# Kernel tuning notes

Hardware: AMD Instinct MI355X
Metric: run time of the kernel (lower is better)

The kernel has to match this reference:

```python
import jax, jax.numpy as jnp
import numpy as np

DIM_MODEL = 2048
DQK = 64
DV = 64
NUM_HEADS = 32
NUM_GROUPS = 8
H_PER_G = NUM_HEADS // NUM_GROUPS
ROPE_THETA = 10000.0
RMS_EPS = 1e-6


def _rope(x):
    # x: [b, g, h, s, d]; rotate-half RoPE over last dim, positions along s.
    d = x.shape[-1]
    s = x.shape[-2]
    inv_freq = 1.0 / (ROPE_THETA ** (jnp.arange(0, d, 2, dtype=jnp.float32) / d))  # [d/2]
    ang = jnp.arange(s, dtype=jnp.float32)[:, None] * inv_freq[None, :]  # [s, d/2]
    cos, sin = jnp.cos(ang), jnp.sin(ang)
    x1, x2 = x[..., : d // 2], x[..., d // 2 :]
    return jnp.concatenate([x1 * cos - x2 * sin, x2 * cos + x1 * sin], axis=-1)


def setup_inputs() -> dict:
    key = jax.random.key(0)
    k1, k2, k3 = jax.random.split(key, 3)
    b, s = 2, 2048
    concat = NUM_HEADS * DQK + NUM_GROUPS * (DQK + DV)  # 3072
    x = jax.random.normal(k1, (b, s, DIM_MODEL), dtype=jnp.float32)
    w_in = jax.random.normal(k2, (concat, DIM_MODEL), dtype=jnp.float32) * (DIM_MODEL ** -0.5)
    w_out = jax.random.normal(k3, (DIM_MODEL, NUM_HEADS * DV), dtype=jnp.float32) * ((NUM_HEADS * DV) ** -0.5)
    rms_w = jnp.ones((DIM_MODEL,), dtype=jnp.float32)
    return {"x": x, "w_in": w_in, "w_out": w_out, "rms_w": rms_w}


def reference(x, w_in, w_out, rms_w):
    b, s, _ = x.shape
    # RMSNorm
    y = x * jax.lax.rsqrt(jnp.mean(x * x, axis=-1, keepdims=True) + RMS_EPS) * rms_w
    # In-projection (Linear, no bias): y @ w_in.T
    y = jnp.einsum('bsm,cm->bsc', y, w_in)
    cq = NUM_HEADS * DQK
    ck = NUM_GROUPS * DQK
    q, k, v = y[..., :cq], y[..., cq:cq + ck], y[..., cq + ck:]
    # q: b s (g h d) -> b g h s d ; k,v: b s (g d) -> b g 1 s d
    q = q.reshape(b, s, NUM_GROUPS, H_PER_G, DQK).transpose(0, 2, 3, 1, 4)
    k = k.reshape(b, s, NUM_GROUPS, DQK).transpose(0, 2, 1, 3)[:, :, None]
    v = v.reshape(b, s, NUM_GROUPS, DV).transpose(0, 2, 1, 3)[:, :, None]
    q = _rope(q)
    k = _rope(k)
    # scores with GQA broadcast over h
    qk = jnp.einsum('bghsd,bgxpd->bghsp', q, k) * (DQK ** -0.5)
    causal = jnp.tril(jnp.ones((s, s), dtype=bool))
    qk = jnp.where(causal, qk, -jnp.inf)
    attn = jax.nn.softmax(qk, axis=-1)
    o = jnp.einsum('bghsp,bgxpd->bghsd', attn, v)  # [b,g,h,s,d]
    o = o.transpose(0, 3, 1, 2, 4).reshape(b, s, NUM_HEADS * DV)
    y = jnp.einsum('bsc,mc->bsm', o, w_out)
    return x + y
```

## Files before the change

kernel.cpp:

```cpp
#include <hip/hip_runtime.h>
#include <hip/hip_bf16.h>

#define TOKENS   4096
#define SEQ      2048
#define DMODEL   2048
#define CONCAT   3072
#define NHEADS   32
#define NGROUPS  8
#define HPERG    4
#define CQ       2048
#define CK       512

typedef __attribute__((ext_vector_type(8))) short bf16x8;
typedef __attribute__((ext_vector_type(4))) float f32x4;

__device__ __forceinline__ ushort f2bf(float f) {
    __hip_bfloat16 h = __float2bfloat16(f);
    return __builtin_bit_cast(ushort, h);
}

#define GLOBAL_TO_LDS16(g, l)                                                  \
    __builtin_amdgcn_global_load_lds(                                          \
        (const __attribute__((address_space(1))) void*)(g),                    \
        (__attribute__((address_space(3))) void*)(l), 16, 0, 0)

__global__ void rmsnorm_kernel(const float* __restrict__ x,
                               const float* __restrict__ w,
                               ushort* __restrict__ y_bf) {
    int t = blockIdx.x;
    const float4* xr = (const float4*)(x + (size_t)t * DMODEL);
    float4 v[2];
    float ss = 0.f;
#pragma unroll
    for (int i = 0; i < 2; i++) {
        v[i] = xr[threadIdx.x + i * 256];
        ss += v[i].x * v[i].x + v[i].y * v[i].y + v[i].z * v[i].z + v[i].w * v[i].w;
    }
#pragma unroll
    for (int off = 32; off >= 1; off >>= 1) ss += __shfl_xor(ss, off);
    __shared__ float red[4];
    int wid = threadIdx.x >> 6;
    if ((threadIdx.x & 63) == 0) red[wid] = ss;
    __syncthreads();
    float total = red[0] + red[1] + red[2] + red[3];
    float scale = rsqrtf(total * (1.0f / DMODEL) + 1e-6f);
    const float4* wr = (const float4*)w;
    ushort4* yr = (ushort4*)(y_bf + (size_t)t * DMODEL);
#pragma unroll
    for (int i = 0; i < 2; i++) {
        int c = threadIdx.x + i * 256;
        float4 wv = wr[c];
        ushort4 o;
        o.x = f2bf(v[i].x * scale * wv.x);
        o.y = f2bf(v[i].y * scale * wv.y);
        o.z = f2bf(v[i].z * scale * wv.z);
        o.w = f2bf(v[i].w * scale * wv.w);
        yr[c] = o;
    }
}

__global__ void pack_bf16_kernel(const float* __restrict__ src,
                                 ushort* __restrict__ dst, int n4) {
    int i = blockIdx.x * 256 + threadIdx.x;
    if (i < n4) {
        float4 v = ((const float4*)src)[i];
        ushort4 o;
        o.x = f2bf(v.x); o.y = f2bf(v.y); o.z = f2bf(v.z); o.w = f2bf(v.w);
        ((ushort4*)dst)[i] = o;
    }
}

#define LGKM(nn) asm volatile("s_waitcnt lgkmcnt(" #nn ")" ::: "memory")
#define VMC(nn)  asm volatile("s_waitcnt vmcnt(" #nn ")" ::: "memory")
#define SBAR()   __builtin_amdgcn_s_barrier()
#define SCHED0() __builtin_amdgcn_sched_barrier(0)
#define PRIO(p)  __builtin_amdgcn_s_setprio(p)

#define RD_A(mh)                                                              \
    _Pragma("unroll") for (int mi = 0; mi < 4; mi++)                          \
    _Pragma("unroll") for (int ks = 0; ks < 2; ks++)                          \
        af[mi][ks] = *(const bf16x8*)(Ab +                                    \
            ((arow0 + (mh) * 64 + mi * 16) * 8 +                              \
             ((ks * 4 + quad) ^ an)) * 8);

#define RD_B(nh)                                                              \
    _Pragma("unroll") for (int ni = 0; ni < NFRAG; ni++)                      \
    _Pragma("unroll") for (int ks = 0; ks < 2; ks++)                          \
        bfr[nh][ni][ks] = *(const bf16x8*)(Bb +                               \
            ((brow0 + (nh) * (16 * NFRAG) + ni * 16) * 8 +                    \
             ((ks * 4 + quad) ^ an)) * 8);

#define MMQ(mh, nh)                                                           \
    _Pragma("unroll") for (int mi = 0; mi < 4; mi++)                          \
    _Pragma("unroll") for (int ni = 0; ni < NFRAG; ni++)                      \
    _Pragma("unroll") for (int ks = 0; ks < 2; ks++)                          \
        acc[(mh) * 4 + mi][(nh) * NFRAG + ni] =                               \
            __builtin_amdgcn_mfma_f32_16x16x32_bf16(af[mi][ks],               \
                bfr[nh][ni][ks], acc[(mh) * 4 + mi][(nh) * NFRAG + ni],       \
                0, 0, 0);

#define ISSUE_HALF(H_)                                                        \
    {                                                                         \
        int H = (H_);                                                         \
        if (H < 4 * NT) {                                                     \
            int t2 = H >> 2, j2 = H & 3;                                      \
            int k0 = t2 << 6;                                                 \
            if (j2 == 0 || j2 == 3) {                                         \
                int half = (j2 == 3);                                         \
                ushort* lb = (ushort*)&As[t2 & 1][0];                         \
                _Pragma("unroll") for (int c = 0; c < 2; c++) {               \
                    int s = w * 2 + c;                                        \
                    int row = (s >> 3) * 128 + half * 64 + (s & 7) * 8;       \
                    const ushort* g = Aptr +                                  \
                        (size_t)(bm + row + l8) * K + k0 + kb8;               \
                    GLOBAL_TO_LDS16(g, lb + row * 64);                        \
                }                                                             \
            } else {                                                          \
                int half = (j2 == 2);                                         \
                ushort* lb = (ushort*)&Bs[t2 & 1][0];                         \
                if constexpr (NFRAG == 2) {                                   \
                    _Pragma("unroll") for (int c = 0; c < 2; c++) {           \
                        int s = w * 2 + c;                                    \
                        int row = (s >> 2) * 64 + half * 32 + (s & 3) * 8;    \
                        const ushort* g = Bptr +                              \
                            (size_t)(bn + row + l8) * K + k0 + kb8;           \
                        GLOBAL_TO_LDS16(g, lb + row * 64);                    \
                    }                                                         \
                } else {                                                      \
                    int row = (w >> 1) * 32 + half * 16 + (w & 1) * 8;        \
                    const ushort* g = Bptr +                                  \
                        (size_t)(bn + row + l8) * K + k0 + kb8;               \
                    GLOBAL_TO_LDS16(g, lb + row * 64);                        \
                }                                                             \
            }                                                                 \
        }                                                                     \
    }

#define VMC_STEADY()                                                          \
    { if constexpr (NFRAG == 2) { VMC(6); } else { VMC(4); } }

#define TILE(t_, BUF)                                                         \
    {                                                                         \
        const ushort* Ab = &As[BUF][0];                                       \
        const ushort* Bb = &Bs[BUF][0];                                       \
                                                \
        RD_A(0); RD_B(0);                                                     \
        ISSUE_HALF(4 * (t_) + 7);                                             \
        LGKM(8);                                                              \
        SBAR(); LGKM(0); SCHED0();                                            \
        PRIO(1); MMQ(0, 0); PRIO(0);                                          \
        SBAR();                                                               \
                                                   \
        RD_B(1);                                                              \
        ISSUE_HALF(4 * (t_) + 8);                                             \
        SBAR(); LGKM(0); SCHED0();                                            \
        PRIO(1); MMQ(0, 1); PRIO(0);                                          \
        SBAR();                                                               \
                                                   \
        RD_A(1);                                                              \
        ISSUE_HALF(4 * (t_) + 9);                                             \
        SBAR(); LGKM(0); SCHED0();                                            \
        PRIO(1); MMQ(1, 0); PRIO(0);                                          \
        SBAR();                                                               \
                           \
        ISSUE_HALF(4 * (t_) + 10);                                            \
        SBAR(); SCHED0();                                                     \
        PRIO(1); MMQ(1, 1); PRIO(0);                                          \
        if ((t_) + 2 < NT)        { VMC_STEADY(); }                           \
        else if ((t_) + 2 == NT)  { VMC(0); }                                 \
        SBAR();                                                               \
    }

template <bool EPILOGUE, int NFRAG>
__global__ __launch_bounds__(512, 2) void gemm_nt_8ph(
        const ushort* __restrict__ Aptr, const ushort* __restrict__ Bptr,
        float* __restrict__ C, const float* __restrict__ X,
        float* __restrict__ OUT, int M, int N, int K) {
    __shared__ __align__(16) ushort As[2][256 * 64];
    __shared__ __align__(16) ushort Bs[2][NFRAG * 128 * 64];

    const int bm = blockIdx.y * 256, bn = blockIdx.x * (128 * NFRAG);
    const int w = threadIdx.x >> 6, lane = threadIdx.x & 63;
    const int n = lane & 15, quad = lane >> 4;
    const int wm = w >> 2, wn = w & 3;
    const int an = n & 7;
    const int l8 = lane >> 3;
    const int kb8 = ((lane & 7) ^ l8) * 8;
    const int arow0 = wm * 128 + n;
    const int brow0 = wn * (32 * NFRAG) + n;
    const int NT = K >> 6;

    f32x4 acc[8][2 * NFRAG] = {};
    bf16x8 af[4][2], bfr[2][NFRAG][2];

    ISSUE_HALF(0); ISSUE_HALF(1); ISSUE_HALF(2); ISSUE_HALF(3);
    ISSUE_HALF(4); ISSUE_HALF(5); ISSUE_HALF(6);
    VMC_STEADY();
    SBAR();

    for (int tt = 0; tt < NT; tt += 2) {
        TILE(tt, 0);
        TILE(tt + 1, 1);
    }

#pragma unroll
    for (int mi = 0; mi < 8; mi++)
#pragma unroll
        for (int ni = 0; ni < 2 * NFRAG; ni++) {
            int row = bm + wm * 128 + mi * 16 + quad * 4;
            int col = bn + wn * (32 * NFRAG) + ni * 16 + n;
#pragma unroll
            for (int r = 0; r < 4; r++) {
                size_t idx = (size_t)(row + r) * N + col;
                float v = acc[mi][ni][r];
                if (EPILOGUE) OUT[idx] = X[idx] + v;
                else          C[idx]   = v;
            }
        }
}

__global__ void pack_qk_kernel(const float* __restrict__ qkv,
                               __hip_bfloat16* __restrict__ Qb,
                               __hip_bfloat16* __restrict__ Kb) {
    int t = blockIdx.x;
    int b = t >> 11, s = t & (SEQ - 1);
    const float* row = qkv + (size_t)t * CONCAT;
    const float LOG2_THETA = 13.287712379549449f;
    const float QSCALE = 0.18033688011112042f;
    for (int i = threadIdx.x; i < CQ + CK; i += 256) {
        int head, d;
        const float* hb;
        if (i < CQ) { head = i >> 6; d = i & 63; hb = row + head * 64; }
        else { head = (i - CQ) >> 6; d = (i - CQ) & 63; hb = row + CQ + head * 64; }
        int j = d & 31;
        float inv = exp2f(-((float)j / 32.0f) * LOG2_THETA);
        float ang = (float)s * inv;
        float c = cosf(ang), sn = sinf(ang);
        float val;
        if (d < 32) val = hb[d] * c - hb[d + 32] * sn;
        else        val = hb[d] * c + hb[d - 32] * sn;
        if (i < CQ) val *= QSCALE;
        __hip_bfloat16 bv = __float2bfloat16(val);
        if (i < CQ) {
            int g = head >> 2, h = head & 3;
            Qb[((size_t)((b * 8 + g) * 4 + h) * SEQ + s) * 64 + d] = bv;
        } else {
            Kb[((size_t)(b * 8 + head) * SEQ + s) * 64 + d] = bv;
        }
    }
}

__global__ void pack_v_kernel(const float* __restrict__ qkv,
                              __hip_bfloat16* __restrict__ Vb) {
    int st = blockIdx.x & 31, bg = blockIdx.x >> 5;
    int b = bg >> 3, g = bg & 7;
    __shared__ float tile[64][65];
    int tid = threadIdx.x;
    int ls = tid >> 6;
    int d = tid & 63;
#pragma unroll
    for (int i = 0; i < 16; i++) {
        int s = st * 64 + i * 4 + ls;
        tile[i * 4 + ls][d] = qkv[(size_t)(b * SEQ + s) * CONCAT + CQ + CK + g * 64 + d];
    }
    __syncthreads();
#pragma unroll
    for (int i = 0; i < 16; i++) {
        int drow = i * 4 + ls;
        int scol = tid & 63;
        Vb[((size_t)(bg * 64 + drow)) * SEQ + st * 64 + scol] =
            __float2bfloat16(tile[scol][drow]);
    }
}

__global__ __launch_bounds__(256) void attn_mfma_kernel(
        const ushort* __restrict__ Qb, const ushort* __restrict__ Kb,
        const ushort* __restrict__ Vb, ushort* __restrict__ o_bf) {
    __shared__ __align__(16) ushort Kl[519 * 8];
    __shared__ __align__(16) ushort Vl[519 * 8];
    __shared__ __align__(16) uint   Pl[4][1056];

    int blk = blockIdx.x;
    int qt  = 15 - (blk >> 6);
    int bgh = blk & 63;
    int h = bgh & 3, g = (bgh >> 2) & 7, b = bgh >> 5;
    int w = threadIdx.x >> 6, lane = threadIdx.x & 63;
    int n = lane & 15, quad = lane >> 4;
    int Q0 = qt * 128;
    int qw = Q0 + w * 32;

    const ushort* Qh  = Qb + (size_t)((b * 8 + g) * 4 + h) * (SEQ * 64);
    const ushort* Kg0 = Kb + (size_t)(b * 8 + g) * (SEQ * 64);
    const ushort* Vg0 = Vb + (size_t)(b * 8 + g) * (64 * SEQ);

    bf16x8 aq[2][2];
#pragma unroll
    for (int qg = 0; qg < 2; qg++)
#pragma unroll
        for (int ks = 0; ks < 2; ks++)
            aq[qg][ks] = *(const bf16x8*)(
                Qh + (size_t)(qw + qg * 16 + n) * 64 + ks * 32 + quad * 8);

    f32x4 od[2][4] = {};
    f32x4 od4[2] = {};

    short onev = (n == 0) ? (short)0x3F80 : (short)0;
    bf16x8 bones = {onev, onev, onev, onev, onev, onev, onev, onev};

    uint* Pw = Pl[w];
    int nkt = qt * 2 + 2;
    for (int kt = 0; kt < nkt; kt++) {
        __syncthreads();
        {
            const ushort* Kg = Kg0 + kt * 64 * 64;
            const ushort* Vg = Vg0 + kt * 64;
#pragma unroll
            for (int rep = 0; rep < 2; rep++) {
                int e = (rep * 256 + threadIdx.x) * 8;
                int key = e >> 6, dblk = (e >> 3) & 7;
                *(bf16x8*)(Kl + (dblk * 65 + key) * 8) = *(const bf16x8*)(Kg + e);
            }
#pragma unroll
            for (int rep = 0; rep < 2; rep++) {
                int e = (rep * 256 + threadIdx.x) * 8;
                int d = e >> 6, kin = e & 63;
                *(bf16x8*)(Vl + ((kin >> 3) * 65 + d) * 8) =
                    *(const bf16x8*)(Vg + (size_t)d * SEQ + kin);
            }
        }
        __syncthreads();

        bool act1 = (kt * 64 <= qw + 31);
        if (!act1) continue;
        bool act0 = (kt * 64 <= qw + 15);

#pragma unroll
        for (int t16k = 0; t16k < 4; t16k++) {
            bf16x8 kf0 = *(const bf16x8*)(Kl + ((0 + quad) * 65 + t16k * 16 + n) * 8);
            bf16x8 kf1 = *(const bf16x8*)(Kl + ((4 + quad) * 65 + t16k * 16 + n) * 8);
            int key0 = kt * 64 + t16k * 16 + quad * 4;
#pragma unroll
            for (int qg = 0; qg < 2; qg++) {
                if (qg == 0 && !act0) continue;
                f32x4 c = {};
                c = __builtin_amdgcn_mfma_f32_16x16x32_bf16(kf0, aq[qg][0], c, 0, 0, 0);
                c = __builtin_amdgcn_mfma_f32_16x16x32_bf16(kf1, aq[qg][1], c, 0, 0, 0);
                int qrow = qw + qg * 16 + n;
                float p[4];
                if (kt * 64 + 63 > qw + qg * 16) {
#pragma unroll
                    for (int r = 0; r < 4; r++)
                        p[r] = (key0 + r <= qrow) ? __builtin_amdgcn_exp2f(c[r]) : 0.f;
                } else {
#pragma unroll
                    for (int r = 0; r < 4; r++)
                        p[r] = __builtin_amdgcn_exp2f(c[r]);
                }
                uint d0 = ((uint)f2bf(p[1]) << 16) | f2bf(p[0]);
                uint d1 = ((uint)f2bf(p[3]) << 16) | f2bf(p[2]);
                int base = ((t16k * 2 + (quad >> 1)) * 33 + qg * 16 + n) * 4
                           + (quad & 1) * 2;
                Pw[base]     = d0;
                Pw[base + 1] = d1;
            }
        }

#pragma unroll
        for (int kb2 = 0; kb2 < 2; kb2++) {
            bf16x8 bv[4];
#pragma unroll
            for (int dt = 0; dt < 4; dt++)
                bv[dt] = *(const bf16x8*)(Vl + ((kb2 * 4 + quad) * 65 + dt * 16 + n) * 8);
#pragma unroll
            for (int qg = 0; qg < 2; qg++) {
                if (qg == 0 && !act0) continue;
                bf16x8 ap = *(const bf16x8*)(
                    (const ushort*)Pw + ((kb2 * 4 + quad) * 33 + qg * 16 + n) * 8);
#pragma unroll
                for (int dt = 0; dt < 4; dt++)
                    od[qg][dt] = __builtin_amdgcn_mfma_f32_16x16x32_bf16(
                        ap, bv[dt], od[qg][dt], 0, 0, 0);
                od4[qg] = __builtin_amdgcn_mfma_f32_16x16x32_bf16(
                    ap, bones, od4[qg], 0, 0, 0);
            }
        }
    }

#pragma unroll
    for (int qg = 0; qg < 2; qg++) {
        float linv[4];
#pragma unroll
        for (int r = 0; r < 4; r++) {
            float lv = __shfl(od4[qg][r], lane & 48);
            linv[r] = __builtin_amdgcn_rcpf(lv);
        }
#pragma unroll
        for (int dt = 0; dt < 4; dt++)
#pragma unroll
            for (int r = 0; r < 4; r++) {
                int q = qw + qg * 16 + quad * 4 + r;
                int col = (g * 4 + h) * 64 + dt * 16 + n;
                o_bf[(size_t)(b * SEQ + q) * DMODEL + col] =
                    f2bf(od[qg][dt][r] * linv[r]);
            }
    }
}

extern "C" void kernel_launch(void* const* d_in, const int* in_sizes, int n_in,
                              void* d_out, int out_size, void* d_ws, size_t ws_size,
                              hipStream_t stream) {
    const float* x     = (const float*)d_in[0];
    const float* w_in  = (const float*)d_in[1];
    const float* w_out = (const float*)d_in[2];
    const float* rms_w = (const float*)d_in[3];
    float* out = (float*)d_out;

    const size_t MB = 1024 * 1024;
    char* ws = (char*)d_ws;
    float*  qkv      = (float*)ws;
    ushort* y_bf     = (ushort*)(ws + 48 * MB);
    ushort* w_in_bf  = (ushort*)(ws + 64 * MB);
    ushort* Qb       = (ushort*)(ws + 48 * MB);
    ushort* Kb       = (ushort*)(ws + 64 * MB);
    ushort* Vb       = (ushort*)(ws + 68 * MB);
    ushort* o_bf     = (ushort*)ws;
    ushort* w_out_bf = (ushort*)(ws + 16 * MB);

    rmsnorm_kernel<<<TOKENS, 256, 0, stream>>>(x, rms_w, y_bf);
    pack_bf16_kernel<<<(CONCAT * DMODEL / 4 + 255) / 256, 256, 0, stream>>>(
        w_in, w_in_bf, CONCAT * DMODEL / 4);

    gemm_nt_8ph<false, 2><<<dim3(CONCAT / 256, TOKENS / 256), 512, 0, stream>>>(
        y_bf, w_in_bf, qkv, nullptr, nullptr, TOKENS, CONCAT, DMODEL);

    pack_qk_kernel<<<TOKENS, 256, 0, stream>>>(qkv, (__hip_bfloat16*)Qb,
                                               (__hip_bfloat16*)Kb);
    pack_v_kernel<<<512, 256, 0, stream>>>(qkv, (__hip_bfloat16*)Vb);
    pack_bf16_kernel<<<(DMODEL * DMODEL / 4 + 255) / 256, 256, 0, stream>>>(
        w_out, w_out_bf, DMODEL * DMODEL / 4);

    attn_mfma_kernel<<<1024, 256, 0, stream>>>(Qb, Kb, Vb, o_bf);

    gemm_nt_8ph<true, 1><<<dim3(DMODEL / 128, TOKENS / 256), 512, 0, stream>>>(
        o_bf, w_out_bf, nullptr, x, out, TOKENS, DMODEL, DMODEL);
}
```

Baseline: 317.8 us.

## Double-buffer attention K/V tiles with async global-to-LDS loads and XOR swizzle

Replaces the synchronous register-staged K/V tile copies in the attention kernel with direct global_load_lds DMA into two LDS buffers, prefetching two tiles ahead so loads overlap the MFMA work. The padded LDS layout is replaced by an XOR-swizzled layout to avoid bank conflicts without padding. LDS use roughly doubles for K/V, and correctness depends on the vmcnt waits and barrier placement.

```diff
diff --git a/kernel.cpp b/kernel.cpp
--- a/kernel.cpp
+++ b/kernel.cpp
@@ -273,11 +273,23 @@
     }
 }
 
+#define AISSUE(kt_, buf_)                                                     \
+    {                                                                         \
+        const ushort* Kg_ = Kg0 + (kt_) * 64 * 64;                            \
+        const ushort* Vg_ = Vg0 + (kt_) * 64;                                 \
+        _Pragma("unroll") for (int r_ = 0; r_ < 2; r_++) {                    \
+            GLOBAL_TO_LDS16(Kg_ + (r_ * 32 + w * 8) * 64 + koff,              \
+                            &Kl[buf_][(r_ * 256 + w * 64) * 8]);              \
+            GLOBAL_TO_LDS16(Vg_ + (size_t)(r_ * 32 + w * 8) * SEQ + voff,     \
+                            &Vl[buf_][(r_ * 256 + w * 64) * 8]);              \
+        }                                                                     \
+    }
+
 __global__ __launch_bounds__(256) void attn_mfma_kernel(
         const ushort* __restrict__ Qb, const ushort* __restrict__ Kb,
         const ushort* __restrict__ Vb, ushort* __restrict__ o_bf) {
-    __shared__ __align__(16) ushort Kl[519 * 8];
-    __shared__ __align__(16) ushort Vl[519 * 8];
+    __shared__ __align__(16) ushort Kl[2][512 * 8];
+    __shared__ __align__(16) ushort Vl[2][512 * 8];
     __shared__ __align__(16) uint   Pl[4][1056];
 
     int blk = blockIdx.x;
@@ -286,8 +298,14 @@
     int h = bgh & 3, g = (bgh >> 2) & 7, b = bgh >> 5;
     int w = threadIdx.x >> 6, lane = threadIdx.x & 63;
     int n = lane & 15, quad = lane >> 4;
+    const int an = n & 7;
     int Q0 = qt * 128;
     int qw = Q0 + w * 32;
+
+    const int l3 = lane >> 3;
+    const int lx = (lane & 7) ^ l3;
+    const int koff = l3 * 64 + lx * 8;
+    const int voff = l3 * SEQ + lx * 8;
 
     const ushort* Qh  = Qb + (size_t)((b * 8 + g) * 4 + h) * (SEQ * 64);
     const ushort* Kg0 = Kb + (size_t)(b * 8 + g) * (SEQ * 64);
@@ -309,81 +327,78 @@
 
     uint* Pw = Pl[w];
     int nkt = qt * 2 + 2;
+
+    AISSUE(0, 0);
+    AISSUE(1, 1);
+
     for (int kt = 0; kt < nkt; kt++) {
-        __syncthreads();
-        {
-            const ushort* Kg = Kg0 + kt * 64 * 64;
-            const ushort* Vg = Vg0 + kt * 64;
-#pragma unroll
-            for (int rep = 0; rep < 2; rep++) {
-                int e = (rep * 256 + threadIdx.x) * 8;
-                int key = e >> 6, dblk = (e >> 3) & 7;
-                *(bf16x8*)(Kl + (dblk * 65 + key) * 8) = *(const bf16x8*)(Kg + e);
+        int buf = kt & 1;
+        if (kt + 1 < nkt) { VMC(4); } else { VMC(0); }
+        SBAR(); SCHED0();
+
+        bool act1 = (kt * 64 <= qw + 31);
+        if (act1) {
+            bool act0 = (kt * 64 <= qw + 15);
+            const ushort* Kb_ = Kl[buf];
+            const ushort* Vb_ = Vl[buf];
+
+#pragma unroll
+            for (int t16k = 0; t16k < 4; t16k++) {
+                int krow = (t16k * 16 + n) * 8;
+                bf16x8 kf0 = *(const bf16x8*)(Kb_ + (krow + (quad ^ an)) * 8);
+                bf16x8 kf1 = *(const bf16x8*)(Kb_ + (krow + ((quad + 4) ^ an)) * 8);
+                int key0 = kt * 64 + t16k * 16 + quad * 4;
+#pragma unroll
+                for (int qg = 0; qg < 2; qg++) {
+                    if (qg == 0 && !act0) continue;
+                    f32x4 c = {};
+                    c = __builtin_amdgcn_mfma_f32_16x16x32_bf16(kf0, aq[qg][0], c, 0, 0, 0);
+                    c = __builtin_amdgcn_mfma_f32_16x16x32_bf16(kf1, aq[qg][1], c, 0, 0, 0);
+                    int qrow = qw + qg * 16 + n;
+                    float p[4];
+                    if (kt * 64 + 63 > qw + qg * 16) {
+#pragma unroll
+                        for (int r = 0; r < 4; r++)
+                            p[r] = (key0 + r <= qrow) ? __builtin_amdgcn_exp2f(c[r]) : 0.f;
+                    } else {
+#pragma unroll
+                        for (int r = 0; r < 4; r++)
+                            p[r] = __builtin_amdgcn_exp2f(c[r]);
+                    }
+                    uint d0 = ((uint)f2bf(p[1]) << 16) | f2bf(p[0]);
+                    uint d1 = ((uint)f2bf(p[3]) << 16) | f2bf(p[2]);
+                    int base = ((t16k * 2 + (quad >> 1)) * 33 + qg * 16 + n) * 4
+                               + (quad & 1) * 2;
+                    Pw[base]     = d0;
+                    Pw[base + 1] = d1;
+                }
             }
-#pragma unroll
-            for (int rep = 0; rep < 2; rep++) {
-                int e = (rep * 256 + threadIdx.x) * 8;
-                int d = e >> 6, kin = e & 63;
-                *(bf16x8*)(Vl + ((kin >> 3) * 65 + d) * 8) =
-                    *(const bf16x8*)(Vg + (size_t)d * SEQ + kin);
+
+#pragma unroll
+            for (int kb2 = 0; kb2 < 2; kb2++) {
+                int kb = kb2 * 4 + quad;
+                bf16x8 bv[4];
+#pragma unroll
+                for (int dt = 0; dt < 4; dt++)
+                    bv[dt] = *(const bf16x8*)(Vb_ +
+                        (((dt * 16 + n) * 8 + (kb ^ an)) * 8));
+#pragma unroll
+                for (int qg = 0; qg < 2; qg++) {
+                    if (qg == 0 && !act0) continue;
+                    bf16x8 ap = *(const bf16x8*)(
+                        (const ushort*)Pw + ((kb2 * 4 + quad) * 33 + qg * 16 + n) * 8);
+#pragma unroll
+                    for (int dt = 0; dt < 4; dt++)
+                        od[qg][dt] = __builtin_amdgcn_mfma_f32_16x16x32_bf16(
+                            ap, bv[dt], od[qg][dt], 0, 0, 0);
+                    od4[qg] = __builtin_amdgcn_mfma_f32_16x16x32_bf16(
+                        ap, bones, od4[qg], 0, 0, 0);
+                }
             }
         }
-        __syncthreads();
-
-        bool act1 = (kt * 64 <= qw + 31);
-        if (!act1) continue;
-        bool act0 = (kt * 64 <= qw + 15);
-
-#pragma unroll
-        for (int t16k = 0; t16k < 4; t16k++) {
-            bf16x8 kf0 = *(const bf16x8*)(Kl + ((0 + quad) * 65 + t16k * 16 + n) * 8);
-            bf16x8 kf1 = *(const bf16x8*)(Kl + ((4 + quad) * 65 + t16k * 16 + n) * 8);
-            int key0 = kt * 64 + t16k * 16 + quad * 4;
-#pragma unroll
-            for (int qg = 0; qg < 2; qg++) {
-                if (qg == 0 && !act0) continue;
-                f32x4 c = {};
-                c = __builtin_amdgcn_mfma_f32_16x16x32_bf16(kf0, aq[qg][0], c, 0, 0, 0);
-                c = __builtin_amdgcn_mfma_f32_16x16x32_bf16(kf1, aq[qg][1], c, 0, 0, 0);
-                int qrow = qw + qg * 16 + n;
-                float p[4];
-                if (kt * 64 + 63 > qw + qg * 16) {
-#pragma unroll
-                    for (int r = 0; r < 4; r++)
-                        p[r] = (key0 + r <= qrow) ? __builtin_amdgcn_exp2f(c[r]) : 0.f;
-                } else {
-#pragma unroll
-                    for (int r = 0; r < 4; r++)
-                        p[r] = __builtin_amdgcn_exp2f(c[r]);
-                }
-                uint d0 = ((uint)f2bf(p[1]) << 16) | f2bf(p[0]);
-                uint d1 = ((uint)f2bf(p[3]) << 16) | f2bf(p[2]);
-                int base = ((t16k * 2 + (quad >> 1)) * 33 + qg * 16 + n) * 4
-                           + (quad & 1) * 2;
-                Pw[base]     = d0;
-                Pw[base + 1] = d1;
-            }
-        }
-
-#pragma unroll
-        for (int kb2 = 0; kb2 < 2; kb2++) {
-            bf16x8 bv[4];
-#pragma unroll
-            for (int dt = 0; dt < 4; dt++)
-                bv[dt] = *(const bf16x8*)(Vl + ((kb2 * 4 + quad) * 65 + dt * 16 + n) * 8);
-#pragma unroll
-            for (int qg = 0; qg < 2; qg++) {
-                if (qg == 0 && !act0) continue;
-                bf16x8 ap = *(const bf16x8*)(
-                    (const ushort*)Pw + ((kb2 * 4 + quad) * 33 + qg * 16 + n) * 8);
-#pragma unroll
-                for (int dt = 0; dt < 4; dt++)
-                    od[qg][dt] = __builtin_amdgcn_mfma_f32_16x16x32_bf16(
-                        ap, bv[dt], od[qg][dt], 0, 0, 0);
-                od4[qg] = __builtin_amdgcn_mfma_f32_16x16x32_bf16(
-                    ap, bones, od4[qg], 0, 0, 0);
-            }
-        }
+
+        SCHED0(); SBAR();
+        if (kt + 2 < nkt) AISSUE(kt + 2, buf);
     }
 
 #pragma unroll
```

New measurement: 317.8 us. About the same (+0.0%).
